# Kernel optimization log

Measured on AMD Instinct MI355X. Metric: run time of the kernel, lower is better.

Reference implementation:

```python
import jax, jax.numpy as jnp
import numpy as np
from math import sqrt

N = 4096      # points
I = 64        # in_channels
H = 64        # hidden_units
O = 64        # out_channels
CUTS = 8
GROUPS = 4
RADIUS = 1.0
BLK = 128     # i-block size for the pairwise interaction (KeOps-style tiling)
EPS = 1e-5


def leaky(x):
    return jnp.where(x >= 0, x, 0.2 * x)


def group_norm(x, w, b):
    # x: (N, C). Matches torch GroupNorm on input (1, C, N):
    # stats per group over (C//GROUPS, N) jointly, affine per channel.
    n, c = x.shape
    xg = x.reshape(n, GROUPS, c // GROUPS)
    mean = xg.mean(axis=(0, 2), keepdims=True)
    var = ((xg - mean) ** 2).mean(axis=(0, 2), keepdims=True)
    xn = ((xg - mean) * jax.lax.rsqrt(var + EPS)).reshape(n, c)
    return xn * w + b


def setup_inputs() -> dict:
    key = jax.random.key(0)
    ks = jax.random.split(key, 16)
    rn = lambda k, s, sc=1.0: jax.random.normal(k, s, jnp.float32) * sc
    # conv MLP init as in the torch module
    A1 = rn(ks[3], (CUTS, 3))                                   # nn.init.normal_
    c1 = jax.random.uniform(ks[4], (CUTS,)) * 0.8 * jnp.sqrt((A1 ** 2).sum(-1))
    A2 = jax.random.uniform(ks[5], (H, CUTS), minval=-1.0 / np.sqrt(CUTS), maxval=1.0 / np.sqrt(CUTS))
    c2 = rn(ks[6], (H,)) * 0.5 * jnp.sqrt((A2 ** 2).sum(-1))
    return {
        "points": rn(ks[0], (N, 3)),
        "nuv": rn(ks[1], (N, 3, 3)),
        "features": rn(ks[2], (N, I)),
        "W_in1": rn(ks[7], (H, I), 1.0 / np.sqrt(I)), "b_in1": jnp.zeros((H,)),
        "W_in2": rn(ks[8], (H, H), 1.0 / np.sqrt(H)), "b_in2": jnp.zeros((H,)),
        "gn_in_w": jnp.ones((H,)), "gn_in_b": jnp.zeros((H,)),
        "A1": A1, "c1": c1, "A2": A2, "c2": c2,
        "W_out1": rn(ks[9], (O, H), 1.0 / np.sqrt(H)), "b_out1": jnp.zeros((O,)),
        "W_out2": rn(ks[10], (O, O), 1.0 / np.sqrt(O)), "b_out2": jnp.zeros((O,)),
        "gn_out_w": jnp.ones((O,)), "gn_out_b": jnp.zeros((O,)),
    }


def reference(points, nuv, features, W_in1, b_in1, W_in2, b_in2, gn_in_w, gn_in_b,
              A1, c1, A2, c2, W_out1, b_out1, W_out2, b_out2, gn_out_w, gn_out_b):
    # 1. net_in MLP + GroupNorm over (1, H, N)
    f = leaky(leaky(features @ W_in1.T + b_in1) @ W_in2.T + b_in2)
    f = group_norm(f, gn_in_w, gn_in_b)                      # (N, H)

    pts = points / (sqrt(2.0) * RADIUS)                      # scaled coords
    n_j = jax.lax.stop_gradient(nuv[:, 0, :])                # j-side normals are detached

    # 2. pairwise quasi-geodesic interaction, tiled over i-blocks.
    # Per-head loop in the original just slices rows of A2/c2 and channels of f;
    # computing the full H-dim conv and reducing is the identical math.
    @jax.checkpoint
    def block(args):
        xi, nuvi = args                                      # (BLK,3), (BLK,3,3)
        diff = pts[None, :, :] - xi[:, None, :]              # (BLK, N, 3) = x_j - x_i
        dot = nuvi[:, 0, :] @ n_j.T                          # (BLK, N) <n_i, n_j>
        d2 = (diff ** 2).sum(-1) * (2.0 - dot) ** 2          # quasi-geodesic d^2
        w = jnp.exp(-d2)                                     # gaussian window w_ij
        X = jnp.einsum('bij,bnj->bni', nuvi, diff)           # P_ij in local basis (BLK,N,3)
        h = jax.nn.relu(jnp.einsum('bni,ci->bnc', X, A1) + c1)   # (BLK,N,CUTS)
        Xc = jax.nn.relu(jnp.einsum('bnc,hc->bnh', h, A2) + c2)  # (BLK,N,H)
        return jnp.einsum('bn,bnh,nh->bh', w, Xc, f)         # sum over j -> (BLK,H)

    out = jax.lax.map(block, (pts.reshape(-1, BLK, 3), nuv.reshape(-1, BLK, 3, 3)))
    out = out.reshape(N, H)

    # 3. net_out MLP + GroupNorm
    g = leaky(leaky(out @ W_out1.T + b_out1) @ W_out2.T + b_out2)
    return group_norm(g, gn_out_w, gn_out_b)                 # (N, O)
```

## Files before the change

### kernel.cpp

```cpp
#include <hip/hip_runtime.h>
#include <hip/hip_bf16.h>
#include <math.h>

#define N_PTS 4096
#define INV_SQRT2 0.70710678118654752440f

typedef float f32x4 __attribute__((ext_vector_type(4)));
typedef float f32x2 __attribute__((ext_vector_type(2)));
typedef short s16x4 __attribute__((ext_vector_type(4)));
typedef short s16x8 __attribute__((ext_vector_type(8)));
typedef _Float16 f16x2 __attribute__((ext_vector_type(2)));

__device__ inline short f2bf(float x) {
    __hip_bfloat16 h = __float2bfloat16(x);
    return __builtin_bit_cast(short, h);
}

__device__ inline unsigned pk_trunc(float hi, float lo) {
    return __builtin_amdgcn_perm(__builtin_bit_cast(unsigned, hi),
                                 __builtin_bit_cast(unsigned, lo),
                                 0x07060302u);
}
__device__ inline unsigned pk_relu(unsigned x) {
    f16x2 v = __builtin_bit_cast(f16x2, x);
    f16x2 z = {(_Float16)0.f, (_Float16)0.f};
    return __builtin_bit_cast(unsigned, __builtin_elementwise_max(v, z));
}
__device__ inline float rfl(float x) {
    return __builtin_bit_cast(float, __builtin_amdgcn_readfirstlane(__builtin_bit_cast(int, x)));
}
__device__ inline f32x2 bc2(float s) { return (f32x2){s, s}; }
__device__ inline f32x2 fma2(f32x2 a, f32x2 b, f32x2 c) {
    return __builtin_elementwise_fma(a, b, c);
}

#if defined(__has_builtin)
#  if __has_builtin(__builtin_amdgcn_mfma_f32_16x16x16bf16_1k)
#    define MFMA16(a, b, c) __builtin_amdgcn_mfma_f32_16x16x16bf16_1k((a), (b), (c), 0, 0, 0)
#    define HAVE_MFMA16 1
#  elif __has_builtin(__builtin_amdgcn_mfma_f32_16x16x16_bf16)
#    define MFMA16(a, b, c) __builtin_amdgcn_mfma_f32_16x16x16_bf16((a), (b), (c), 0, 0, 0)
#    define HAVE_MFMA16 1
#  endif
#endif
#ifndef HAVE_MFMA16
__device__ inline f32x4 mfma16_asm(s16x4 a, s16x4 b, f32x4 c) {
    asm volatile("s_nop 1\n\tv_mfma_f32_16x16x16_bf16 %0, %1, %2, %0"
                 : "+v"(c) : "v"(a), "v"(b));
    return c;
}
#  define MFMA16(a, b, c) mfma16_asm((a), (b), (c))
#endif

#define MFMA32(a, b, c) __builtin_amdgcn_mfma_f32_16x16x32_bf16((a), (b), (c), 0, 0, 0)

__global__ __launch_bounds__(256) void mlp_gn_kernel(
    const float* __restrict__ inp, int extra,
    const float* __restrict__ W1, const float* __restrict__ b1,
    const float* __restrict__ W2, const float* __restrict__ b2,
    float* __restrict__ pre_out, float* __restrict__ partials)
{
    __shared__ float in_s[4][64];
    __shared__ float h1_s[4][64];
    __shared__ float red_s[4][8];

    const int tid = threadIdx.x;
    const int lane = tid & 63;
    const int wid = tid >> 6;
    const int n0 = blockIdx.x * 4;

    float xin = inp[n0 * 64 + tid];
    for (int s = 1; s <= extra; ++s)
        xin += inp[(size_t)s * (N_PTS * 64) + n0 * 64 + tid];
    in_s[wid][lane] = xin;
    __syncthreads();

    const int c = lane;
    float h = b1[c];
#pragma unroll
    for (int k4 = 0; k4 < 16; ++k4) {
        float4 wv = *(const float4*)&W1[c * 64 + k4 * 4];
        h = fmaf(in_s[wid][k4*4+0], wv.x, h);
        h = fmaf(in_s[wid][k4*4+1], wv.y, h);
        h = fmaf(in_s[wid][k4*4+2], wv.z, h);
        h = fmaf(in_s[wid][k4*4+3], wv.w, h);
    }
    h = (h >= 0.f) ? h : 0.2f * h;
    h1_s[wid][c] = h;
    __syncthreads();

    float g = b2[c];
#pragma unroll
    for (int k4 = 0; k4 < 16; ++k4) {
        float4 wv = *(const float4*)&W2[c * 64 + k4 * 4];
        g = fmaf(h1_s[wid][k4*4+0], wv.x, g);
        g = fmaf(h1_s[wid][k4*4+1], wv.y, g);
        g = fmaf(h1_s[wid][k4*4+2], wv.z, g);
        g = fmaf(h1_s[wid][k4*4+3], wv.w, g);
    }
    g = (g >= 0.f) ? g : 0.2f * g;
    pre_out[n0 * 64 + tid] = g;

    float v = g, v2 = g * g;
#pragma unroll
    for (int m = 1; m < 16; m <<= 1) {
        v  += __shfl_xor(v,  m, 64);
        v2 += __shfl_xor(v2, m, 64);
    }
    if ((lane & 15) == 0) {
        int grp = lane >> 4;
        red_s[wid][grp * 2 + 0] = v;
        red_s[wid][grp * 2 + 1] = v2;
    }
    __syncthreads();
    if (tid < 8) {
        int grp = tid >> 1, which = tid & 1;
        float s = red_s[0][grp*2+which] + red_s[1][grp*2+which]
                + red_s[2][grp*2+which] + red_s[3][grp*2+which];
        partials[blockIdx.x * 8 + grp * 2 + which] = s;
    }
}

__global__ __launch_bounds__(256) void finalize_kernel(
    const float* __restrict__ partials, int nblocks,
    const float* __restrict__ gw, const float* __restrict__ gb,
    float* __restrict__ ss)
{
    __shared__ float red[8][32];
    __shared__ float mean_s[4], inv_s[4];
    const int t = threadIdx.x;
    const int s = t >> 5, slot = t & 31;
    float acc = 0.f;
    for (int b = slot; b < nblocks; b += 32) acc += partials[b * 8 + s];
    red[s][slot] = acc;
    __syncthreads();
    if (t < 8) {
        float v = 0.f;
#pragma unroll
        for (int k = 0; k < 32; ++k) v += red[t][k];
        red[t][0] = v;
    }
    __syncthreads();
    if (t < 4) {
        float S = red[t * 2][0], SS = red[t * 2 + 1][0];
        const float cnt = (float)N_PTS * 16.f;
        float mean = S / cnt;
        float var = SS / cnt - mean * mean;
        mean_s[t] = mean;
        inv_s[t] = rsqrtf(var + 1e-5f);
    }
    __syncthreads();
    if (t < 64) {
        int grp = t >> 4;
        float sc = gw[t] * inv_s[grp];
        ss[t] = sc;
        ss[64 + t] = gb[t] - mean_s[grp] * sc;
    }
}

__global__ __launch_bounds__(256) void fnt_kernel(
    const float* __restrict__ f_pre, const float* __restrict__ ss,
    short* __restrict__ fn_sw,
    const float* __restrict__ points, const float* __restrict__ nuv,
    float* __restrict__ ptn4)
{
    const int h = blockIdx.x >> 4;
    const int j = ((blockIdx.x & 15) << 8) + threadIdx.x;
    float v = f_pre[j * 64 + h] * ss[h] + ss[64 + h];
    const int t = j >> 6, jj = j & 63;
    const int jsub = jj >> 4, g = (jj >> 2) & 3, r = jj & 3;
    const int jp = jsub >> 1, lo = jsub & 1;
    const int ht = h >> 4, hl = h & 15;
    const int unit = ((t * 2 + jp) * 4 + ht) * 64 + hl * 4 + g;
    fn_sw[unit * 8 + lo * 4 + r] = f2bf(v);

    if (blockIdx.x < 16) {
        const int pt = blockIdx.x * 256 + threadIdx.x;
        float sx = points[pt*3+0] * INV_SQRT2;
        float sy = points[pt*3+1] * INV_SQRT2;
        float sz = points[pt*3+2] * INV_SQRT2;
        float nx = nuv[pt*9+0], ny = nuv[pt*9+1], nz = nuv[pt*9+2];
        *(float4*)&ptn4[pt*8 + 0] = (float4){sx, sy, sz, 0.f};
        *(float4*)&ptn4[pt*8 + 4] = (float4){nx, ny, nz, 0.f};
    }
}

__global__ __launch_bounds__(256, 4) void pairwise_kernel(
    const float* __restrict__ nuv,
    const float* __restrict__ ptn4,
    const short* __restrict__ fn_sw,
    const float* __restrict__ A1, const float* __restrict__ c1,
    const float* __restrict__ A2, const float* __restrict__ c2,
    float* __restrict__ out_part, int nt, int jshift)
{
    __shared__ __align__(16) short P_s[8][768];

    const int tid = threadIdx.x;
    const int l = tid & 63;
    const int wid = tid >> 6;
    const int g = l >> 4;
    const int hl = l & 15;

    const int js = blockIdx.x & ((1 << jshift) - 1);
    const int ig = blockIdx.x >> jshift;
    const int i0 = ig * 8 + wid * 2;
    const int tmask = nt - 1;

    f32x2 nv2[9];
#pragma unroll
    for (int k = 0; k < 9; ++k)
        nv2[k] = (f32x2){rfl(nuv[i0 * 9 + k]), rfl(nuv[(i0 + 1) * 9 + k])};
    const f32x2 pix2 = (f32x2){rfl(ptn4[i0*8+0]), rfl(ptn4[(i0+1)*8+0])};
    const f32x2 piy2 = (f32x2){rfl(ptn4[i0*8+1]), rfl(ptn4[(i0+1)*8+1])};
    const f32x2 piz2 = (f32x2){rfl(ptn4[i0*8+2]), rfl(ptn4[(i0+1)*8+2])};

    float a1v[8][3], c1v[8];
#pragma unroll
    for (int cc = 0; cc < 8; ++cc) {
        a1v[cc][0] = A1[cc*3+0]; a1v[cc][1] = A1[cc*3+1]; a1v[cc][2] = A1[cc*3+2];
        c1v[cc] = c1[cc];
    }

    s16x4 A2sB[4];
#pragma unroll
    for (int ht = 0; ht < 4; ++ht) {
        const int h = ht * 16 + hl;
        s16x4 v;
#pragma unroll
        for (int r = 0; r < 4; ++r) {
            const int cc = 4 * g + r;
            float val = (cc < 8) ? A2[h*8 + cc] : ((cc == 8) ? c2[h] : 0.f);
            v[r] = f2bf(val);
        }
        A2sB[ht] = v;
    }

    f32x4 acc0[4], acc1[4];
#pragma unroll
    for (int ht = 0; ht < 4; ++ht) {
        acc0[ht] = (f32x4){0.f, 0.f, 0.f, 0.f};
        acc1[ht] = (f32x4){0.f, 0.f, 0.f, 0.f};
    }
    const f32x4 Zzero = (f32x4){0.f, 0.f, 0.f, 0.f};

    const int laneoff = (hl * 4 + g) * 8;
    const short* fnb = fn_sw + (size_t)(js * nt) * 4096;
    const float* pbase = ptn4 + (size_t)(js * nt) * 512;

    float4 pj_c = *(const float4*)&pbase[l * 8];
    float4 nj_c = *(const float4*)&pbase[l * 8 + 4];

    for (int t = 0; t < nt; ++t) {
        const short* bt = fnb + t * 4096;
        s16x8 Fv[2][4];
#pragma unroll
        for (int jp = 0; jp < 2; ++jp)
#pragma unroll
            for (int ht = 0; ht < 4; ++ht)
                Fv[jp][ht] = *(const s16x8*)(bt + (jp * 4 + ht) * 512 + laneoff);

        const int tn = (t + 1) & tmask;
        float4 pj_n = *(const float4*)&pbase[(tn * 64 + l) * 8];
        float4 nj_n = *(const float4*)&pbase[(tn * 64 + l) * 8 + 4];

        {
            f32x2 dx = bc2(pj_c.x) - pix2;
            f32x2 dy = bc2(pj_c.y) - piy2;
            f32x2 dz = bc2(pj_c.z) - piz2;
            f32x2 s1 = fma2(dz, dz, fma2(dy, dy, dx * dx));
            f32x2 dt = fma2(nv2[2], bc2(nj_c.z),
                       fma2(nv2[1], bc2(nj_c.y), nv2[0] * bc2(nj_c.x)));
            f32x2 t2 = bc2(2.f) - dt;
            f32x2 d2 = (s1 * t2) * t2;
            float w0 = __expf(-d2[0]);
            float w1 = __expf(-d2[1]);
            f32x2 wp = (f32x2){w0, w1};
            f32x2 X0 = fma2(nv2[2], dz, fma2(nv2[1], dy, nv2[0] * dx));
            f32x2 X1 = fma2(nv2[5], dz, fma2(nv2[4], dy, nv2[3] * dx));
            f32x2 X2 = fma2(nv2[8], dz, fma2(nv2[7], dy, nv2[6] * dx));

            f32x2 hv[8];
#pragma unroll
            for (int cc = 0; cc < 8; ++cc) {
                f32x2 tt = fma2(bc2(a1v[cc][2]), X2,
                           fma2(bc2(a1v[cc][1]), X1,
                           fma2(bc2(a1v[cc][0]), X0, bc2(c1v[cc]))));
                hv[cc] = tt * wp;
            }
            {
                int2 ra, rb, rc;
                ra.x = (int)pk_relu(pk_trunc(hv[1][0], hv[0][0]));
                ra.y = (int)pk_relu(pk_trunc(hv[3][0], hv[2][0]));
                rb.x = (int)pk_relu(pk_trunc(hv[5][0], hv[4][0]));
                rb.y = (int)pk_relu(pk_trunc(hv[7][0], hv[6][0]));
                rc.x = (int)(__builtin_bit_cast(unsigned, w0) >> 16);
                rc.y = 0;
                short* rp = &P_s[wid * 2 + 0][l * 12];
                *(int2*)(rp + 0) = ra;
                *(int2*)(rp + 4) = rb;
                *(int2*)(rp + 8) = rc;
            }
            {
                int2 ra, rb, rc;
                ra.x = (int)pk_relu(pk_trunc(hv[1][1], hv[0][1]));
                ra.y = (int)pk_relu(pk_trunc(hv[3][1], hv[2][1]));
                rb.x = (int)pk_relu(pk_trunc(hv[5][1], hv[4][1]));
                rb.y = (int)pk_relu(pk_trunc(hv[7][1], hv[6][1]));
                rc.x = (int)(__builtin_bit_cast(unsigned, w1) >> 16);
                rc.y = 0;
                short* rp = &P_s[wid * 2 + 1][l * 12];
                *(int2*)(rp + 0) = ra;
                *(int2*)(rp + 4) = rb;
                *(int2*)(rp + 8) = rc;
            }
        }

#pragma unroll
        for (int jp = 0; jp < 2; ++jp) {
            const int j0 = (jp * 2 + 0) * 16 + hl;
            const int j1 = (jp * 2 + 1) * 16 + hl;
            const s16x4 Af00 = *(const s16x4*)&P_s[wid*2+0][j0 * 12 + 4 * g];
            const s16x4 Af01 = *(const s16x4*)&P_s[wid*2+0][j1 * 12 + 4 * g];
            const s16x4 Af10 = *(const s16x4*)&P_s[wid*2+1][j0 * 12 + 4 * g];
            const s16x4 Af11 = *(const s16x4*)&P_s[wid*2+1][j1 * 12 + 4 * g];
#pragma unroll
            for (int ht = 0; ht < 4; ++ht) {
                const s16x8 Fvv = Fv[jp][ht];
                f32x4 Za = MFMA16(Af00, A2sB[ht], Zzero);
                f32x4 Zb = MFMA16(Af01, A2sB[ht], Zzero);
                int4 b0;
                b0.x = (int)pk_relu(pk_trunc(Za[1], Za[0]));
                b0.y = (int)pk_relu(pk_trunc(Za[3], Za[2]));
                b0.z = (int)pk_relu(pk_trunc(Zb[1], Zb[0]));
                b0.w = (int)pk_relu(pk_trunc(Zb[3], Zb[2]));
                acc0[ht] = MFMA32(Fvv, __builtin_bit_cast(s16x8, b0), acc0[ht]);
                f32x4 Zc = MFMA16(Af10, A2sB[ht], Zzero);
                f32x4 Zd = MFMA16(Af11, A2sB[ht], Zzero);
                int4 b1;
                b1.x = (int)pk_relu(pk_trunc(Zc[1], Zc[0]));
                b1.y = (int)pk_relu(pk_trunc(Zc[3], Zc[2]));
                b1.z = (int)pk_relu(pk_trunc(Zd[1], Zd[0]));
                b1.w = (int)pk_relu(pk_trunc(Zd[3], Zd[2]));
                acc1[ht] = MFMA32(Fvv, __builtin_bit_cast(s16x8, b1), acc1[ht]);
            }
        }
        pj_c = pj_n; nj_c = nj_n;
    }

    asm volatile("s_nop 7\n\ts_nop 7" ::: );

    if (g == (hl >> 2)) {
        const int r = hl & 3;
        float* ob = out_part + (size_t)js * (N_PTS * 64);
#pragma unroll
        for (int ht = 0; ht < 4; ++ht) {
            float v0 = (r == 0) ? acc0[ht][0] : (r == 1) ? acc0[ht][1]
                     : (r == 2) ? acc0[ht][2] : acc0[ht][3];
            float v1 = (r == 0) ? acc1[ht][0] : (r == 1) ? acc1[ht][1]
                     : (r == 2) ? acc1[ht][2] : acc1[ht][3];
            ob[(i0 + 0) * 64 + ht * 16 + hl] = v0;
            ob[(i0 + 1) * 64 + ht * 16 + hl] = v1;
        }
    }
}

__global__ __launch_bounds__(256) void apply_kernel(
    const float* __restrict__ pre, const float* __restrict__ ss,
    float* __restrict__ out)
{
    int idx = blockIdx.x * 256 + threadIdx.x;
    int c = idx & 63;
    out[idx] = pre[idx] * ss[c] + ss[64 + c];
}

extern "C" void kernel_launch(void* const* d_in, const int* in_sizes, int n_in,
                              void* d_out, int out_size, void* d_ws, size_t ws_size,
                              hipStream_t stream) {
    const float* points   = (const float*)d_in[0];
    const float* nuv      = (const float*)d_in[1];
    const float* features = (const float*)d_in[2];
    const float* W_in1    = (const float*)d_in[3];
    const float* b_in1    = (const float*)d_in[4];
    const float* W_in2    = (const float*)d_in[5];
    const float* b_in2    = (const float*)d_in[6];
    const float* gn_in_w  = (const float*)d_in[7];
    const float* gn_in_b  = (const float*)d_in[8];
    const float* A1       = (const float*)d_in[9];
    const float* c1       = (const float*)d_in[10];
    const float* A2       = (const float*)d_in[11];
    const float* c2       = (const float*)d_in[12];
    const float* W_out1   = (const float*)d_in[13];
    const float* b_out1   = (const float*)d_in[14];
    const float* W_out2   = (const float*)d_in[15];
    const float* b_out2   = (const float*)d_in[16];
    const float* gn_out_w = (const float*)d_in[17];
    const float* gn_out_b = (const float*)d_in[18];

    const size_t MB = 1048576;
    const int JS = (ws_size >= 5 * MB) ? 4 : 2;
    const int jshift = (JS == 4) ? 2 : 1;
    const int nt = 64 / JS;
    const size_t op_bytes = (size_t)JS * N_PTS * 64 * 4;

    char* ws = (char*)d_ws;
    float* out_part = (float*)(ws + 0);
    float* f_pre    = (float*)(ws + 0);
    float* g_pre    = (float*)(ws + 0);
    short* fn_sw    = (short*)(ws + op_bytes);
    float* ptn4     = (float*)(ws + op_bytes + 524288);
    char*  tail     = ws + op_bytes + 524288 + 131072;
    float* part_in  = (float*)(tail);
    float* part_out = (float*)(tail + 32768);
    float* ss_in    = (float*)(tail + 65536);
    float* ss_out   = (float*)(tail + 66048);

    float* outp = (float*)d_out;

    mlp_gn_kernel<<<1024, 256, 0, stream>>>(features, 0, W_in1, b_in1,
                                            W_in2, b_in2, f_pre, part_in);
    finalize_kernel<<<1, 256, 0, stream>>>(part_in, 1024, gn_in_w, gn_in_b, ss_in);
    fnt_kernel<<<1024, 256, 0, stream>>>(f_pre, ss_in, fn_sw, points, nuv, ptn4);

    pairwise_kernel<<<512 * JS, 256, 0, stream>>>(nuv, ptn4, fn_sw,
                                                  A1, c1, A2, c2, out_part,
                                                  nt, jshift);

    mlp_gn_kernel<<<1024, 256, 0, stream>>>(out_part, JS - 1, W_out1, b_out1,
                                            W_out2, b_out2, g_pre, part_out);
    finalize_kernel<<<1, 256, 0, stream>>>(part_out, 1024, gn_out_w, gn_out_b, ss_out);

    apply_kernel<<<1024, 256, 0, stream>>>(g_pre, ss_out, outp);
}
```

Baseline: 166.5 us.

## Double-buffer per-wave LDS tile to overlap next-tile geometry with MFMA phase

The per-pair geometry and first-layer computation for tile t+1 is now done before the MFMA stage of tile t, writing into a second LDS buffer. The shared P_s array doubles in size and point prefetch moves two tiles ahead. This software pipelining lets VALU/transcendental work interleave with matrix-core work within a wave. It costs extra LDS per block, which may reduce occupancy, and adds register pressure.

```diff
diff --git a/kernel.cpp b/kernel.cpp
--- a/kernel.cpp
+++ b/kernel.cpp
@@ -193,7 +193,7 @@
     const float* __restrict__ A2, const float* __restrict__ c2,
     float* __restrict__ out_part, int nt, int jshift)
 {
-    __shared__ __align__(16) short P_s[8][768];
+    __shared__ __align__(16) short P_s[16][768];
 
     const int tid = threadIdx.x;
     const int l = tid & 63;
@@ -247,10 +247,69 @@
     const short* fnb = fn_sw + (size_t)(js * nt) * 4096;
     const float* pbase = ptn4 + (size_t)(js * nt) * 512;
 
-    float4 pj_c = *(const float4*)&pbase[l * 8];
-    float4 nj_c = *(const float4*)&pbase[l * 8 + 4];
+    auto phase1 = [&](int buf, float4 pj, float4 nj) {
+        f32x2 dx = bc2(pj.x) - pix2;
+        f32x2 dy = bc2(pj.y) - piy2;
+        f32x2 dz = bc2(pj.z) - piz2;
+        f32x2 s1 = fma2(dz, dz, fma2(dy, dy, dx * dx));
+        f32x2 dt = fma2(nv2[2], bc2(nj.z),
+                   fma2(nv2[1], bc2(nj.y), nv2[0] * bc2(nj.x)));
+        f32x2 t2 = bc2(2.f) - dt;
+        f32x2 d2 = (s1 * t2) * t2;
+        float w0 = __expf(-d2[0]);
+        float w1 = __expf(-d2[1]);
+        f32x2 wp = (f32x2){w0, w1};
+        f32x2 X0 = fma2(nv2[2], dz, fma2(nv2[1], dy, nv2[0] * dx));
+        f32x2 X1 = fma2(nv2[5], dz, fma2(nv2[4], dy, nv2[3] * dx));
+        f32x2 X2 = fma2(nv2[8], dz, fma2(nv2[7], dy, nv2[6] * dx));
+
+        f32x2 hv[8];
+#pragma unroll
+        for (int cc = 0; cc < 8; ++cc) {
+            f32x2 tt = fma2(bc2(a1v[cc][2]), X2,
+                       fma2(bc2(a1v[cc][1]), X1,
+                       fma2(bc2(a1v[cc][0]), X0, bc2(c1v[cc]))));
+            hv[cc] = tt * wp;
+        }
+        {
+            int2 ra, rb, rc;
+            ra.x = (int)pk_relu(pk_trunc(hv[1][0], hv[0][0]));
+            ra.y = (int)pk_relu(pk_trunc(hv[3][0], hv[2][0]));
+            rb.x = (int)pk_relu(pk_trunc(hv[5][0], hv[4][0]));
+            rb.y = (int)pk_relu(pk_trunc(hv[7][0], hv[6][0]));
+            rc.x = (int)(__builtin_bit_cast(unsigned, w0) >> 16);
+            rc.y = 0;
+            short* rp = &P_s[wid * 4 + 0 + buf][l * 12];
+            *(int2*)(rp + 0) = ra;
+            *(int2*)(rp + 4) = rb;
+            *(int2*)(rp + 8) = rc;
+        }
+        {
+            int2 ra, rb, rc;
+            ra.x = (int)pk_relu(pk_trunc(hv[1][1], hv[0][1]));
+            ra.y = (int)pk_relu(pk_trunc(hv[3][1], hv[2][1]));
+            rb.x = (int)pk_relu(pk_trunc(hv[5][1], hv[4][1]));
+            rb.y = (int)pk_relu(pk_trunc(hv[7][1], hv[6][1]));
+            rc.x = (int)(__builtin_bit_cast(unsigned, w1) >> 16);
+            rc.y = 0;
+            short* rp = &P_s[wid * 4 + 2 + buf][l * 12];
+            *(int2*)(rp + 0) = ra;
+            *(int2*)(rp + 4) = rb;
+            *(int2*)(rp + 8) = rc;
+        }
+    };
+
+    {
+        float4 pj0 = *(const float4*)&pbase[l * 8];
+        float4 nj0 = *(const float4*)&pbase[l * 8 + 4];
+        phase1(0, pj0, nj0);
+    }
+    float4 pj_c = *(const float4*)&pbase[((1 & tmask) * 64 + l) * 8];
+    float4 nj_c = *(const float4*)&pbase[((1 & tmask) * 64 + l) * 8 + 4];
 
     for (int t = 0; t < nt; ++t) {
+        const int buf = t & 1;
+
         const short* bt = fnb + t * 4096;
         s16x8 Fv[2][4];
 #pragma unroll
@@ -259,70 +318,20 @@
             for (int ht = 0; ht < 4; ++ht)
                 Fv[jp][ht] = *(const s16x8*)(bt + (jp * 4 + ht) * 512 + laneoff);
 
-        const int tn = (t + 1) & tmask;
+        const int tn = (t + 2) & tmask;
         float4 pj_n = *(const float4*)&pbase[(tn * 64 + l) * 8];
         float4 nj_n = *(const float4*)&pbase[(tn * 64 + l) * 8 + 4];
 
-        {
-            f32x2 dx = bc2(pj_c.x) - pix2;
-            f32x2 dy = bc2(pj_c.y) - piy2;
-            f32x2 dz = bc2(pj_c.z) - piz2;
-            f32x2 s1 = fma2(dz, dz, fma2(dy, dy, dx * dx));
-            f32x2 dt = fma2(nv2[2], bc2(nj_c.z),
-                       fma2(nv2[1], bc2(nj_c.y), nv2[0] * bc2(nj_c.x)));
-            f32x2 t2 = bc2(2.f) - dt;
-            f32x2 d2 = (s1 * t2) * t2;
-            float w0 = __expf(-d2[0]);
-            float w1 = __expf(-d2[1]);
-            f32x2 wp = (f32x2){w0, w1};
-            f32x2 X0 = fma2(nv2[2], dz, fma2(nv2[1], dy, nv2[0] * dx));
-            f32x2 X1 = fma2(nv2[5], dz, fma2(nv2[4], dy, nv2[3] * dx));
-            f32x2 X2 = fma2(nv2[8], dz, fma2(nv2[7], dy, nv2[6] * dx));
-
-            f32x2 hv[8];
-#pragma unroll
-            for (int cc = 0; cc < 8; ++cc) {
-                f32x2 tt = fma2(bc2(a1v[cc][2]), X2,
-                           fma2(bc2(a1v[cc][1]), X1,
-                           fma2(bc2(a1v[cc][0]), X0, bc2(c1v[cc]))));
-                hv[cc] = tt * wp;
-            }
-            {
-                int2 ra, rb, rc;
-                ra.x = (int)pk_relu(pk_trunc(hv[1][0], hv[0][0]));
-                ra.y = (int)pk_relu(pk_trunc(hv[3][0], hv[2][0]));
-                rb.x = (int)pk_relu(pk_trunc(hv[5][0], hv[4][0]));
-                rb.y = (int)pk_relu(pk_trunc(hv[7][0], hv[6][0]));
-                rc.x = (int)(__builtin_bit_cast(unsigned, w0) >> 16);
-                rc.y = 0;
-                short* rp = &P_s[wid * 2 + 0][l * 12];
-                *(int2*)(rp + 0) = ra;
-                *(int2*)(rp + 4) = rb;
-                *(int2*)(rp + 8) = rc;
-            }
-            {
-                int2 ra, rb, rc;
-                ra.x = (int)pk_relu(pk_trunc(hv[1][1], hv[0][1]));
-                ra.y = (int)pk_relu(pk_trunc(hv[3][1], hv[2][1]));
-                rb.x = (int)pk_relu(pk_trunc(hv[5][1], hv[4][1]));
-                rb.y = (int)pk_relu(pk_trunc(hv[7][1], hv[6][1]));
-                rc.x = (int)(__builtin_bit_cast(unsigned, w1) >> 16);
-                rc.y = 0;
-                short* rp = &P_s[wid * 2 + 1][l * 12];
-                *(int2*)(rp + 0) = ra;
-                *(int2*)(rp + 4) = rb;
-                *(int2*)(rp + 8) = rc;
-            }
-        }
+        if (t < nt - 1) phase1(buf ^ 1, pj_c, nj_c);
 
 #pragma unroll
         for (int jp = 0; jp < 2; ++jp) {
             const int j0 = (jp * 2 + 0) * 16 + hl;
             const int j1 = (jp * 2 + 1) * 16 + hl;
-            const s16x4 Af00 = *(const s16x4*)&P_s[wid*2+0][j0 * 12 + 4 * g];
-            const s16x4 Af01 = *(const s16x4*)&P_s[wid*2+0][j1 * 12 + 4 * g];
-            const s16x4 Af10 = *(const s16x4*)&P_s[wid*2+1][j0 * 12 + 4 * g];
-            const s16x4 Af11 = *(const s16x4*)&P_s[wid*2+1][j1 * 12 + 4 * g];
+            const s16x4 Af00 = *(const s16x4*)&P_s[wid*4 + 0 + buf][j0 * 12 + 4 * g];
+            const s16x4 Af01 = *(const s16x4*)&P_s[wid*4 + 0 + buf][j1 * 12 + 4 * g];
+            const s16x4 Af10 = *(const s16x4*)&P_s[wid*4 + 2 + buf][j0 * 12 + 4 * g];
+            const s16x4 Af11 = *(const s16x4*)&P_s[wid*4 + 2 + buf][j1 * 12 + 4 * g];
 #pragma unroll
             for (int ht = 0; ht < 4; ++ht) {
                 const s16x8 Fvv = Fv[jp][ht];
```

Result: slower. 175.0 us (+5.1%).
